# Kernel optimization log

Measured on AMD Instinct MI355X. Metric: run time of the kernel, lower is better.

The kernel has to match this reference:

```python
import jax, jax.numpy as jnp
import numpy as np
from jax import lax

KS = 7; KC = 64; S = 31; B = 1; H = 128; W = 128; ITERS = 3
LAM = 0.1   # Softshrink lambda
EPS = 1e-5  # BatchNorm eps


def conv2d(x, w, b):
    # x: [N,C,H,W], w: [O,C,kh,kw], b: [O]; stride 1, SAME padding (ks odd)
    y = lax.conv_general_dilated(x, w, (1, 1), 'SAME',
                                 dimension_numbers=('NCHW', 'OIHW', 'NCHW'))
    return y + b[None, :, None, None]


def band_conv(x5, w, b):
    # x5: [S,B,C,H,W] -> apply shared conv per band by merging S into batch
    s, bb, c, h, ww = x5.shape
    y = conv2d(x5.reshape(s * bb, c, h, ww), w, b)
    return y.reshape(s, bb, -1, h, ww)


def softshrink(x):
    return jnp.sign(x) * jnp.maximum(jnp.abs(x) - LAM, 0.0)


def setup_inputs() -> dict:
    key = jax.random.key(0)
    ks = jax.random.split(key, 12)
    sc = 0.05
    inputs = jax.random.normal(ks[0], (B, S, H, W), jnp.float32)
    W_fe   = jax.random.normal(ks[1], (KC, 1, KS, KS), jnp.float32) * sc
    b_fe   = jax.random.normal(ks[2], (KC,), jnp.float32) * sc
    W_enc  = jax.random.normal(ks[3], (ITERS, KC, 1, KS, KS), jnp.float32) * sc
    b_enc  = jax.random.normal(ks[4], (ITERS, KC), jnp.float32) * sc
    W_dec  = jax.random.normal(ks[5], (ITERS, 1, KC, KS, KS), jnp.float32) * sc
    b_dec  = jax.random.normal(ks[6], (ITERS, 1), jnp.float32) * sc
    W_last = jax.random.normal(ks[7], (1, KC, KS, KS), jnp.float32) * sc
    b_last = jax.random.normal(ks[8], (1,), jnp.float32) * sc
    W_z    = jax.random.normal(ks[9], (ITERS, KC, KC, KS, KS), jnp.float32) * sc
    b_z    = jax.random.normal(ks[10], (ITERS, KC), jnp.float32) * sc
    bn_gamma = jnp.ones((ITERS, KC), jnp.float32)
    bn_beta  = jnp.zeros((ITERS, KC), jnp.float32)
    return dict(inputs=inputs, W_fe=W_fe, b_fe=b_fe, W_enc=W_enc, b_enc=b_enc,
                W_dec=W_dec, b_dec=b_dec, W_last=W_last, b_last=b_last,
                W_z=W_z, b_z=b_z, bn_gamma=bn_gamma, bn_beta=bn_beta)


def reference(inputs, W_fe, b_fe, W_enc, b_enc, W_dec, b_dec,
              W_last, b_last, W_z, b_z, bn_gamma, bn_beta):
    # inputs: [B, S, H, W]; treat each band as [B,1,H,W]
    x = jnp.transpose(inputs, (1, 0, 2, 3))[:, :, None]  # [S,B,1,H,W]
    # initial sparse code per band (shared first encoder + softshrink)
    csc = softshrink(band_conv(x, W_fe, b_fe))            # [S,B,KC,H,W]

    for it in range(ITERS):
        lyr = it % ITERS  # cycle(range(_layers)) with _layers == ista_iters
        # per-band ISTA step (vectorized over bands)
        res = x - band_conv(csc, W_dec[lyr], b_dec[lyr])
        tmp = softshrink(csc + band_conv(res, W_enc[lyr], b_enc[lyr]))
        # GRU-style gate: sigmoid(BN(conv(tmp))); BN uses per-call (per-band)
        # batch statistics over (B,H,W) per channel, matching training mode
        zpre = band_conv(tmp, W_z[lyr], b_z[lyr])          # [S,B,KC,H,W]
        mu = jnp.mean(zpre, axis=(1, 3, 4), keepdims=True)
        var = jnp.var(zpre, axis=(1, 3, 4), keepdims=True)
        zn = (zpre - mu) * lax.rsqrt(var + EPS)
        g = bn_gamma[lyr][None, None, :, None, None]
        be = bn_beta[lyr][None, None, :, None, None]
        z = jax.nn.sigmoid(zn * g + be)
        # direction alternates: even iters sweep bands forward, odd backward
        fwd = (it % 2 == 0)
        t = tmp if fwd else tmp[::-1]
        zz = z if fwd else z[::-1]

        def step(carry, inp):
            ti, zi = inp
            new = zi * carry + (1.0 - zi) * ti
            return new, new

        _, ys = lax.scan(step, t[0], (t[1:], zz[1:]))
        seq = jnp.concatenate([t[:1], ys], axis=0)
        csc = seq if fwd else seq[::-1]

    out = band_conv(csc, W_last, b_last)[:, :, 0]  # [S,B,H,W]
    outputs = jnp.transpose(out, (1, 0, 2, 3))     # [B,S,H,W]
    return (csc, outputs)
```

## Files before the change

kernel.cpp:

```cpp
#include <hip/hip_runtime.h>
#include <hip/hip_bf16.h>
#include <math.h>

#define S31   31
#define KC    64
#define KS    7
#define KK    49
#define IMG   128
#define HW    16384
#define LAM   0.1f
#define BNEPS 1e-5f

#define PLSTRIDE 3872

#define TW    32
#define TH    8
#define DTW   38
#define DTH   14
#define DTILE 532

typedef __attribute__((ext_vector_type(8))) short  frag8;
typedef __attribute__((ext_vector_type(4))) float  facc4;

static __device__ __forceinline__ short f2bf(float f) {
    union { float f; unsigned u; } x; x.f = f;
    unsigned r = x.u + 0x7fffu + ((x.u >> 16) & 1u);
    return (short)(r >> 16);
}

__global__ void reorder_weights(const float* __restrict__ Wz,
                                const float* __restrict__ Wenc,
                                const float* __restrict__ Wfe,
                                short* __restrict__ wz_frag,
                                float* __restrict__ wenc_r,
                                float* __restrict__ wfe_r,
                                float* __restrict__ pstats) {
    int tid = blockIdx.x * 256 + threadIdx.x;
    const int NZ = 3 * KK * 4096;
    const int NE = 3 * KK * KC;
    const int NF = KK * KC;
    const int NP = 2 * S31 * KC;
    if (tid < NZ) {
        int j    = tid & 7;
        int lane = (tid >> 3) & 63;
        int og   = (tid >> 9) & 3;
        int ks   = (tid >> 11) & 1;
        int rem  = tid >> 12;
        int khkw = rem % KK;
        int lyr  = rem / KK;
        int ic = ks * 32 + ((lane >> 4) << 3) + j;
        int oc = (og << 4) + (lane & 15);
        float w = Wz[(((size_t)lyr * KC + oc) * KC + ic) * KK + khkw];
        wz_frag[tid] = f2bf(w);
    } else if (tid < NZ + NE) {
        int t = tid - NZ;
        int oc = t & 63;
        int kk = t >> 6;
        int k  = kk % KK;
        int lyr = kk / KK;
        wenc_r[t] = Wenc[((size_t)lyr * KC + oc) * KK + k];
    } else if (tid < NZ + NE + NF) {
        int t = tid - NZ - NE;
        int oc = t & 63;
        int k  = t >> 6;
        wfe_r[t] = Wfe[oc * KK + k];
    } else if (tid < NZ + NE + NF + NP) {
        pstats[tid - NZ - NE - NF] = 0.f;
    }
}

__global__ __launch_bounds__(256) void conv1to64(
        const float* __restrict__ src,
        const float* __restrict__ wr,
        const float* __restrict__ bias,
        const float* __restrict__ addsrc,
        float* __restrict__ dst,
        short* __restrict__ dst_t)
{
    int s    = blockIdx.y;
    int half = blockIdx.x & 1;
    int tile = blockIdx.x >> 1;
    int t    = threadIdx.x;
    int tx = t & 31, ty = t >> 5;
    int w0 = (tile & 3) << 5, h0 = (tile >> 2) << 3;

    __shared__ float t_s[DTILE];
    const float* sp = src + (size_t)s * HW;
    for (int i = threadIdx.x; i < DTILE; i += 256) {
        int r = i / DTW, c = i - r * DTW;
        int hh = h0 - 3 + r, ww = w0 - 3 + c;
        t_s[i] = (hh >= 0 && hh < IMG && ww >= 0 && ww < IMG) ? sp[hh * IMG + ww] : 0.f;
    }
    __syncthreads();

    int pix = (h0 + ty) * IMG + (w0 + tx);
    size_t base = ((size_t)s * KC + half * 32) * HW + pix;

    float addv[32];
    if (addsrc) {
#pragma unroll
        for (int i = 0; i < 32; i++) addv[i] = addsrc[base + (size_t)i * HW];
    } else {
#pragma unroll
        for (int i = 0; i < 32; i++) addv[i] = 0.f;
    }
    __builtin_amdgcn_sched_barrier(0);

    float acc[32];
#pragma unroll
    for (int i = 0; i < 32; i++) acc[i] = 0.f;

    const float* wrh = wr + half * 32;
#pragma unroll 1
    for (int kh = 0; kh < KS; kh++) {
#pragma unroll
        for (int kw = 0; kw < KS; kw++) {
            float v = t_s[(ty + kh) * DTW + tx + kw];
            const float* wk = wrh + (kh * KS + kw) * KC;
#pragma unroll
            for (int i = 0; i < 32; i++) acc[i] += v * wk[i];
        }
    }

    short* tb = dst_t ? (dst_t + (((size_t)half * S31 + s) * HW + pix) * 32) : nullptr;
#pragma unroll
    for (int g = 0; g < 4; g++) {
        frag8 vv;
#pragma unroll
        for (int j = 0; j < 8; j++) {
            int i = g * 8 + j;
            float v = acc[i] + bias[half * 32 + i];
            v += addv[i];
            v = (v > LAM) ? (v - LAM) : ((v < -LAM) ? (v + LAM) : 0.f);
            dst[base + (size_t)i * HW] = v;
            vv[j] = f2bf(v);
        }
        if (tb) *(frag8*)(tb + g * 8) = vv;
    }
}

#define ICB   4
#define CHUNK (ICB * DTILE)

__global__ __launch_bounds__(256) void conv64to1(
        const float* __restrict__ src,
        const float* __restrict__ w,
        const float* __restrict__ bias,
        const float* __restrict__ xsub,
        float* __restrict__ dst)
{
    int s    = blockIdx.y;
    int tile = blockIdx.x;
    int tx = threadIdx.x & 31, ty = threadIdx.x >> 5;
    int w0 = (tile & 3) << 5, h0 = (tile >> 2) << 3;

    __shared__ float t_s[2][CHUNK];

    int  goff[9];
    bool okf[9];
#pragma unroll
    for (int r = 0; r < 9; r++) {
        int j = threadIdx.x + r * 256;
        if (j < CHUNK) {
            int plane = j / DTILE, p = j - plane * DTILE;
            int rr = p / DTW, cc = p - rr * DTW;
            int hh = h0 - 3 + rr, ww = w0 - 3 + cc;
            bool inb = (hh >= 0 && hh < IMG && ww >= 0 && ww < IMG);
            goff[r] = plane * HW + (inb ? (hh * IMG + ww) : 0);
            okf[r]  = inb;
        }
    }

    const float* sbase = src + (size_t)s * KC * HW;

    float ldv[9];
#pragma unroll
    for (int r = 0; r < 9; r++)
        if (threadIdx.x + r * 256 < CHUNK)
            ldv[r] = okf[r] ? sbase[goff[r]] : 0.f;
#pragma unroll
    for (int r = 0; r < 9; r++)
        if (threadIdx.x + r * 256 < CHUNK)
            t_s[0][threadIdx.x + r * 256] = ldv[r];

    float acc = 0.f;
    __syncthreads();

#pragma unroll 1
    for (int blk = 0; blk < 16; blk++) {
        int cur = blk & 1;
        if (blk < 15) {
            const float* nb = sbase + (size_t)(blk + 1) * ICB * HW;
#pragma unroll
            for (int r = 0; r < 9; r++)
                if (threadIdx.x + r * 256 < CHUNK)
                    ldv[r] = okf[r] ? nb[goff[r]] : 0.f;
        }
        __builtin_amdgcn_sched_barrier(0);
#pragma unroll
        for (int pl = 0; pl < ICB; pl++) {
            int ic = blk * ICB + pl;
            const float* wk = w + ic * KK;
            const float* ts = &t_s[cur][pl * DTILE];
#pragma unroll 1
            for (int kh = 0; kh < KS; kh++) {
#pragma unroll
                for (int kw = 0; kw < KS; kw++)
                    acc += ts[(ty + kh) * DTW + tx + kw] * wk[kh * KS + kw];
            }
        }
        __syncthreads();
        if (blk < 15) {
#pragma unroll
            for (int r = 0; r < 9; r++)
                if (threadIdx.x + r * 256 < CHUNK)
                    t_s[cur ^ 1][threadIdx.x + r * 256] = ldv[r];
            __syncthreads();
        }
    }

    float v = acc + bias[0];
    int pix = (h0 + ty) * IMG + (w0 + tx);
    if (xsub) v = xsub[(size_t)s * HW + pix] - v;
    dst[(size_t)s * HW + pix] = v;
}

__global__ __launch_bounds__(512, 4) void conv_z_mfma(
        const short* __restrict__ srcT,
        const short* __restrict__ wfrag,
        const float* __restrict__ bias,
        float* __restrict__ dst,
        float* __restrict__ pstats)
{
    __shared__ __align__(16) short a_s[4 * PLSTRIDE];

    int s    = blockIdx.y;
    int tile = blockIdx.x;
    int h0 = (tile >> 3) << 4, w0 = (tile & 7) << 4;
    int tid  = threadIdx.x;
    int wave = tid >> 6, lane = tid & 63;
    int q = lane >> 4, m = lane & 15;

    facc4 acc[2][4];
#pragma unroll
    for (int i = 0; i < 2; i++)
#pragma unroll
        for (int j = 0; j < 4; j++)
            acc[i][j] = (facc4){0.f, 0.f, 0.f, 0.f};

#pragma unroll 1
    for (int pass = 0; pass < 2; ++pass) {
        if (pass) __syncthreads();

        const frag8* brow = (const frag8*)wfrag + (pass * 4) * 64 + lane;
        frag8 c0 = brow[0], c1 = brow[64], c2 = brow[128], c3 = brow[192];

        const short* tsrc = srcT + ((size_t)pass * S31 + s) * HW * 32;
        {
            int p = tid;
            if (p < 484) {
                int r = p / 22, c = p - r * 22;
                int hh = h0 - 3 + r, ww = w0 - 3 + c;
                bool ok = (hh >= 0 && hh < IMG && ww >= 0 && ww < IMG);
                const short* px = tsrc + (size_t)(ok ? (hh * IMG + ww) : 0) * 32;
                short* dp = a_s + p * 8;
#pragma unroll
                for (int c4 = 0; c4 < 4; c4++) {
                    frag8 v;
                    if (ok) v = *(const frag8*)(px + (c4 << 3));
                    else    v = (frag8)(short)0;
                    *(frag8*)(dp + c4 * PLSTRIDE) = v;
                }
            }
        }
        __syncthreads();

        const short* arow = a_s + q * PLSTRIDE + (wave * 2 * 22 + m) * 8;

#pragma unroll 1
        for (int kh = 0; kh < 7; ++kh) {
#pragma unroll
            for (int kw = 0; kw < 7; ++kw) {
                const frag8* bn = brow + (kw == 6 ? 7 : (kw + 1)) * 512;
                frag8 n0 = bn[0], n1 = bn[64], n2 = bn[128], n3 = bn[192];
                frag8 a0 = *(const frag8*)(arow + (0 * 22 + kw) * 8);
                frag8 a1 = *(const frag8*)(arow + (1 * 22 + kw) * 8);
                acc[0][0] = __builtin_amdgcn_mfma_f32_16x16x32_bf16(a0, c0, acc[0][0], 0, 0, 0);
                acc[0][1] = __builtin_amdgcn_mfma_f32_16x16x32_bf16(a0, c1, acc[0][1], 0, 0, 0);
                acc[0][2] = __builtin_amdgcn_mfma_f32_16x16x32_bf16(a0, c2, acc[0][2], 0, 0, 0);
                acc[0][3] = __builtin_amdgcn_mfma_f32_16x16x32_bf16(a0, c3, acc[0][3], 0, 0, 0);
                acc[1][0] = __builtin_amdgcn_mfma_f32_16x16x32_bf16(a1, c0, acc[1][0], 0, 0, 0);
                acc[1][1] = __builtin_amdgcn_mfma_f32_16x16x32_bf16(a1, c1, acc[1][1], 0, 0, 0);
                acc[1][2] = __builtin_amdgcn_mfma_f32_16x16x32_bf16(a1, c2, acc[1][2], 0, 0, 0);
                acc[1][3] = __builtin_amdgcn_mfma_f32_16x16x32_bf16(a1, c3, acc[1][3], 0, 0, 0);
                c0 = n0; c1 = n1; c2 = n2; c3 = n3;
            }
            arow += 22 * 8;
            brow += 7 * 512;
        }
    }

    int prow = h0 + wave * 2;
#pragma unroll
    for (int og = 0; og < 4; og++) {
        int oc = og * 16 + m;
        float bb = bias[oc];
        float s1 = 0.f, s2 = 0.f;
#pragma unroll
        for (int pg = 0; pg < 2; pg++) {
            float* dp = dst + ((size_t)s * KC + oc) * HW
                            + (size_t)(prow + pg) * IMG + w0 + q * 4;
            float4 v;
            v.x = acc[pg][og][0] + bb;
            v.y = acc[pg][og][1] + bb;
            v.z = acc[pg][og][2] + bb;
            v.w = acc[pg][og][3] + bb;
            s1 += v.x + v.y + v.z + v.w;
            s2 += v.x * v.x + v.y * v.y + v.z * v.z + v.w * v.w;
            *(float4*)dp = v;
        }
        s1 += __shfl_xor(s1, 16, 64); s2 += __shfl_xor(s2, 16, 64);
        s1 += __shfl_xor(s1, 32, 64); s2 += __shfl_xor(s2, 32, 64);
        if (q == 0) {
            atomicAdd(&pstats[(s * KC + oc) * 2],     s1);
            atomicAdd(&pstats[(s * KC + oc) * 2 + 1], s2);
        }
    }
}

__global__ __launch_bounds__(64) void bn_finalize(
        float* __restrict__ pstats,
        float* __restrict__ stats)
{
    int i = blockIdx.x * 64 + threadIdx.x;
    if (i < S31 * KC) {
        float s1 = pstats[i * 2], s2 = pstats[i * 2 + 1];
        pstats[i * 2] = 0.f;
        pstats[i * 2 + 1] = 0.f;
        float mu  = s1 * (1.f / HW);
        float var = s2 * (1.f / HW) - mu * mu;
        if (var < 0.f) var = 0.f;
        stats[i * 2]     = mu;
        stats[i * 2 + 1] = rsqrtf(var + BNEPS);
    }
}

__global__ __launch_bounds__(256) void band_scan(
        const float* __restrict__ tmp,
        const float* __restrict__ zpre,
        const float* __restrict__ stats,
        const float* __restrict__ gamma,
        const float* __restrict__ beta,
        float* __restrict__ csc,
        int fwd)
{
    int idx = blockIdx.x * 256 + threadIdx.x;
    int c = idx >> 14;
    float g = gamma[c], be = beta[c];
    float prev = 0.f;
    for (int step = 0; step < S31; step++) {
        int s = fwd ? step : (S31 - 1 - step);
        size_t off = (size_t)s * KC * HW + idx;
        float t  = tmp[off];
        float zp = zpre[off];
        float mu = stats[(s * KC + c) * 2];
        float rs = stats[(s * KC + c) * 2 + 1];
        float zn = (zp - mu) * rs * g + be;
        float z  = 1.f / (1.f + expf(-zn));
        float cur = (step == 0) ? t : (z * prev + (1.f - z) * t);
        csc[off] = cur;
        prev = cur;
    }
}

extern "C" void kernel_launch(void* const* d_in, const int* in_sizes, int n_in,
                              void* d_out, int out_size, void* d_ws, size_t ws_size,
                              hipStream_t stream) {
    const float* x      = (const float*)d_in[0];
    const float* W_fe   = (const float*)d_in[1];
    const float* b_fe   = (const float*)d_in[2];
    const float* W_enc  = (const float*)d_in[3];
    const float* b_enc  = (const float*)d_in[4];
    const float* W_dec  = (const float*)d_in[5];
    const float* b_dec  = (const float*)d_in[6];
    const float* W_last = (const float*)d_in[7];
    const float* b_last = (const float*)d_in[8];
    const float* W_z    = (const float*)d_in[9];
    const float* b_z    = (const float*)d_in[10];
    const float* bn_g   = (const float*)d_in[11];
    const float* bn_b   = (const float*)d_in[12];

    float* out     = (float*)d_out;
    float* csc     = out;
    float* outputs = out + (size_t)S31 * KC * HW;

    char* ws = (char*)d_ws;
    float* tmp     = (float*)ws; ws += (size_t)S31 * KC * HW * 4;
    float* zpre    = (float*)ws; ws += (size_t)S31 * KC * HW * 4;
    float* res     = (float*)ws; ws += (size_t)S31 * HW * 4;
    float* stats   = (float*)ws; ws += (size_t)S31 * KC * 2 * 4;
    float* pstats  = (float*)ws; ws += (size_t)S31 * KC * 2 * 4;
    short* wz_frag = (short*)ws; ws += ((size_t)3 * KK * 4096 + 4096) * 2;
    float* wenc_r  = (float*)ws; ws += (size_t)3 * KK * KC * 4;
    float* wfe_r   = (float*)ws; ws += (size_t)KK * KC * 4;
    short* tmp_t   = (short*)ws; ws += (size_t)2 * S31 * HW * 32 * 2;

    {
        int total = 3 * KK * 4096 + 3 * KK * KC + KK * KC + 2 * S31 * KC;
        reorder_weights<<<(total + 255) / 256, 256, 0, stream>>>(
            W_z, W_enc, W_fe, wz_frag, wenc_r, wfe_r, pstats);
    }

    dim3 gconv(64, S31);
    dim3 gconv2(128, S31);

    conv1to64<<<gconv2, 256, 0, stream>>>(x, wfe_r, b_fe, nullptr, csc, nullptr);

    for (int it = 0; it < 3; it++) {
        int lyr = it;
        conv64to1<<<gconv, 256, 0, stream>>>(
            csc, W_dec + (size_t)lyr * KC * KK, b_dec + lyr, x, res);
        conv1to64<<<gconv2, 256, 0, stream>>>(
            res, wenc_r + (size_t)lyr * KK * KC, b_enc + (size_t)lyr * KC, csc,
            tmp, tmp_t);
        conv_z_mfma<<<gconv, 512, 0, stream>>>(
            tmp_t, wz_frag + (size_t)lyr * KK * 4096, b_z + (size_t)lyr * KC,
            zpre, pstats);
        bn_finalize<<<S31, 64, 0, stream>>>(pstats, stats);
        band_scan<<<(KC * HW) / 256, 256, 0, stream>>>(
            tmp, zpre, stats, bn_g + (size_t)lyr * KC, bn_b + (size_t)lyr * KC,
            csc, (it % 2 == 0) ? 1 : 0);
    }

    conv64to1<<<gconv, 256, 0, stream>>>(csc, W_last, b_last, nullptr, outputs);
}
```

Measured before the change: 2.053 ms.

## Give each wave four pixel rows in conv_z MFMA and prefetch A fragments

The z-gate convolution block shrinks from 512 to 256 threads, and each wave now computes a 4x4 grid of 16x16 MFMA tiles (four pixel rows by four channel groups) instead of 2x4. Each weight fragment loaded from global memory is therefore reused across twice as many rows, and both the LDS A fragments and the B fragments are software-pipelined one step ahead. The aim is fewer weight loads per MFMA and better latency hiding. In exchange the kernel needs more accumulator and prefetch registers, and the launch bound drops to 3 blocks per CU with fewer waves per block, which lowers occupancy.

```diff
diff --git a/kernel.cpp b/kernel.cpp
--- a/kernel.cpp
+++ b/kernel.cpp
@@ -225,7 +225,7 @@
     dst[(size_t)s * HW + pix] = v;
 }
 
-__global__ __launch_bounds__(512, 4) void conv_z_mfma(
+__global__ __launch_bounds__(256, 3) void conv_z_mfma(
         const short* __restrict__ srcT,
         const short* __restrict__ wfrag,
         const float* __restrict__ bias,
@@ -241,9 +241,9 @@
     int wave = tid >> 6, lane = tid & 63;
     int q = lane >> 4, m = lane & 15;
 
-    facc4 acc[2][4];
-#pragma unroll
-    for (int i = 0; i < 2; i++)
+    facc4 acc[4][4];
+#pragma unroll
+    for (int i = 0; i < 4; i++)
 #pragma unroll
         for (int j = 0; j < 4; j++)
             acc[i][j] = (facc4){0.f, 0.f, 0.f, 0.f};
@@ -252,12 +252,10 @@
     for (int pass = 0; pass < 2; ++pass) {
         if (pass) __syncthreads();
 
-        const frag8* brow = (const frag8*)wfrag + (pass * 4) * 64 + lane;
-        frag8 c0 = brow[0], c1 = brow[64], c2 = brow[128], c3 = brow[192];
-
         const short* tsrc = srcT + ((size_t)pass * S31 + s) * HW * 32;
-        {
-            int p = tid;
+#pragma unroll
+        for (int rep = 0; rep < 2; rep++) {
+            int p = tid + rep * 256;
             if (p < 484) {
                 int r = p / 22, c = p - r * 22;
                 int hh = h0 - 3 + r, ww = w0 - 3 + c;
@@ -275,39 +273,60 @@
         }
         __syncthreads();
 
-        const short* arow = a_s + q * PLSTRIDE + (wave * 2 * 22 + m) * 8;
+        const short* arow = a_s + q * PLSTRIDE + (wave * 4 * 22 + m) * 8;
+        const frag8* brow = (const frag8*)wfrag + (pass * 4) * 64 + lane;
+
+        frag8 ca0 = *(const frag8*)(arow + (0 * 22) * 8);
+        frag8 ca1 = *(const frag8*)(arow + (1 * 22) * 8);
+        frag8 ca2 = *(const frag8*)(arow + (2 * 22) * 8);
+        frag8 ca3 = *(const frag8*)(arow + (3 * 22) * 8);
+        frag8 cb0 = brow[0], cb1 = brow[64], cb2 = brow[128], cb3 = brow[192];
 
 #pragma unroll 1
         for (int kh = 0; kh < 7; ++kh) {
+            const short* arow_n = (kh < 6) ? (arow + 22 * 8) : arow;
 #pragma unroll
             for (int kw = 0; kw < 7; ++kw) {
-                const frag8* bn = brow + (kw == 6 ? 7 : (kw + 1)) * 512;
-                frag8 n0 = bn[0], n1 = bn[64], n2 = bn[128], n3 = bn[192];
-                frag8 a0 = *(const frag8*)(arow + (0 * 22 + kw) * 8);
-                frag8 a1 = *(const frag8*)(arow + (1 * 22 + kw) * 8);
-                acc[0][0] = __builtin_amdgcn_mfma_f32_16x16x32_bf16(a0, c0, acc[0][0], 0, 0, 0);
-                acc[0][1] = __builtin_amdgcn_mfma_f32_16x16x32_bf16(a0, c1, acc[0][1], 0, 0, 0);
-                acc[0][2] = __builtin_amdgcn_mfma_f32_16x16x32_bf16(a0, c2, acc[0][2], 0, 0, 0);
-                acc[0][3] = __builtin_amdgcn_mfma_f32_16x16x32_bf16(a0, c3, acc[0][3], 0, 0, 0);
-                acc[1][0] = __builtin_amdgcn_mfma_f32_16x16x32_bf16(a1, c0, acc[1][0], 0, 0, 0);
-                acc[1][1] = __builtin_amdgcn_mfma_f32_16x16x32_bf16(a1, c1, acc[1][1], 0, 0, 0);
-                acc[1][2] = __builtin_amdgcn_mfma_f32_16x16x32_bf16(a1, c2, acc[1][2], 0, 0, 0);
-                acc[1][3] = __builtin_amdgcn_mfma_f32_16x16x32_bf16(a1, c3, acc[1][3], 0, 0, 0);
-                c0 = n0; c1 = n1; c2 = n2; c3 = n3;
+                const short* an = (kw < 6) ? arow : arow_n;
+                const int koff = (kw < 6) ? (kw + 1) : 0;
+                const frag8* bn = brow + (kw + 1) * 512;
+                frag8 na0 = *(const frag8*)(an + (0 * 22 + koff) * 8);
+                frag8 na1 = *(const frag8*)(an + (1 * 22 + koff) * 8);
+                frag8 na2 = *(const frag8*)(an + (2 * 22 + koff) * 8);
+                frag8 na3 = *(const frag8*)(an + (3 * 22 + koff) * 8);
+                frag8 nb0 = bn[0], nb1 = bn[64], nb2 = bn[128], nb3 = bn[192];
+                acc[0][0] = __builtin_amdgcn_mfma_f32_16x16x32_bf16(ca0, cb0, acc[0][0], 0, 0, 0);
+                acc[0][1] = __builtin_amdgcn_mfma_f32_16x16x32_bf16(ca0, cb1, acc[0][1], 0, 0, 0);
+                acc[0][2] = __builtin_amdgcn_mfma_f32_16x16x32_bf16(ca0, cb2, acc[0][2], 0, 0, 0);
+                acc[0][3] = __builtin_amdgcn_mfma_f32_16x16x32_bf16(ca0, cb3, acc[0][3], 0, 0, 0);
+                acc[1][0] = __builtin_amdgcn_mfma_f32_16x16x32_bf16(ca1, cb0, acc[1][0], 0, 0, 0);
+                acc[1][1] = __builtin_amdgcn_mfma_f32_16x16x32_bf16(ca1, cb1, acc[1][1], 0, 0, 0);
+                acc[1][2] = __builtin_amdgcn_mfma_f32_16x16x32_bf16(ca1, cb2, acc[1][2], 0, 0, 0);
+                acc[1][3] = __builtin_amdgcn_mfma_f32_16x16x32_bf16(ca1, cb3, acc[1][3], 0, 0, 0);
+                acc[2][0] = __builtin_amdgcn_mfma_f32_16x16x32_bf16(ca2, cb0, acc[2][0], 0, 0, 0);
+                acc[2][1] = __builtin_amdgcn_mfma_f32_16x16x32_bf16(ca2, cb1, acc[2][1], 0, 0, 0);
+                acc[2][2] = __builtin_amdgcn_mfma_f32_16x16x32_bf16(ca2, cb2, acc[2][2], 0, 0, 0);
+                acc[2][3] = __builtin_amdgcn_mfma_f32_16x16x32_bf16(ca2, cb3, acc[2][3], 0, 0, 0);
+                acc[3][0] = __builtin_amdgcn_mfma_f32_16x16x32_bf16(ca3, cb0, acc[3][0], 0, 0, 0);
+                acc[3][1] = __builtin_amdgcn_mfma_f32_16x16x32_bf16(ca3, cb1, acc[3][1], 0, 0, 0);
+                acc[3][2] = __builtin_amdgcn_mfma_f32_16x16x32_bf16(ca3, cb2, acc[3][2], 0, 0, 0);
+                acc[3][3] = __builtin_amdgcn_mfma_f32_16x16x32_bf16(ca3, cb3, acc[3][3], 0, 0, 0);
+                ca0 = na0; ca1 = na1; ca2 = na2; ca3 = na3;
+                cb0 = nb0; cb1 = nb1; cb2 = nb2; cb3 = nb3;
             }
             arow += 22 * 8;
             brow += 7 * 512;
         }
     }
 
-    int prow = h0 + wave * 2;
+    int prow = h0 + wave * 4;
 #pragma unroll
     for (int og = 0; og < 4; og++) {
         int oc = og * 16 + m;
         float bb = bias[oc];
         float s1 = 0.f, s2 = 0.f;
 #pragma unroll
-        for (int pg = 0; pg < 2; pg++) {
+        for (int pg = 0; pg < 4; pg++) {
             float* dp = dst + ((size_t)s * KC + oc) * HW
                             + (size_t)(prow + pg) * IMG + w0 + q * 4;
             float4 v;
@@ -423,7 +442,7 @@
         conv1to64<<<gconv2, 256, 0, stream>>>(
             res, wenc_r + (size_t)lyr * KK * KC, b_enc + (size_t)lyr * KC, csc,
             tmp, tmp_t);
-        conv_z_mfma<<<gconv, 512, 0, stream>>>(
+        conv_z_mfma<<<gconv, 256, 0, stream>>>(
             tmp_t, wz_frag + (size_t)lyr * KK * 4096, b_z + (size_t)lyr * KC,
             zpre, pstats);
         bn_finalize<<<S31, 64, 0, stream>>>(pstats, stats);
```

After: 1.749 ms. 1.17x faster.

## Give each wave four output rows in z-conv and reuse A fragments across kh

Applied to the files above, without the earlier changes.

The z-gate MFMA conv now runs 256 threads per block, and each wave computes four output rows instead of two, doubling the accumulators. The loop order is swapped to kw-outer, kh-inner, so A fragments slide through a four-register window with one new LDS load per kh. B weight fragments are prefetched two steps ahead. This cuts LDS reads and weight loads per MFMA, at the cost of higher register pressure and fewer waves per block.

```diff
diff --git a/kernel.cpp b/kernel.cpp
--- a/kernel.cpp
+++ b/kernel.cpp
@@ -225,7 +225,7 @@
     dst[(size_t)s * HW + pix] = v;
 }
 
-__global__ __launch_bounds__(512, 4) void conv_z_mfma(
+__global__ __launch_bounds__(256, 3) void conv_z_mfma(
         const short* __restrict__ srcT,
         const short* __restrict__ wfrag,
         const float* __restrict__ bias,
@@ -241,9 +241,9 @@
     int wave = tid >> 6, lane = tid & 63;
     int q = lane >> 4, m = lane & 15;
 
-    facc4 acc[2][4];
-#pragma unroll
-    for (int i = 0; i < 2; i++)
+    facc4 acc[4][4];
+#pragma unroll
+    for (int i = 0; i < 4; i++)
 #pragma unroll
         for (int j = 0; j < 4; j++)
             acc[i][j] = (facc4){0.f, 0.f, 0.f, 0.f};
@@ -252,12 +252,10 @@
     for (int pass = 0; pass < 2; ++pass) {
         if (pass) __syncthreads();
 
-        const frag8* brow = (const frag8*)wfrag + (pass * 4) * 64 + lane;
-        frag8 c0 = brow[0], c1 = brow[64], c2 = brow[128], c3 = brow[192];
-
         const short* tsrc = srcT + ((size_t)pass * S31 + s) * HW * 32;
-        {
-            int p = tid;
+#pragma unroll
+        for (int rep = 0; rep < 2; rep++) {
+            int p = tid + rep * 256;
             if (p < 484) {
                 int r = p / 22, c = p - r * 22;
                 int hh = h0 - 3 + r, ww = w0 - 3 + c;
@@ -275,16 +273,30 @@
         }
         __syncthreads();
 
-        const short* arow = a_s + q * PLSTRIDE + (wave * 2 * 22 + m) * 8;
+        const frag8* bbase = (const frag8*)wfrag + (pass * 4) * 64 + lane;
 
 #pragma unroll 1
-        for (int kh = 0; kh < 7; ++kh) {
-#pragma unroll
-            for (int kw = 0; kw < 7; ++kw) {
-                const frag8* bn = brow + (kw == 6 ? 7 : (kw + 1)) * 512;
-                frag8 n0 = bn[0], n1 = bn[64], n2 = bn[128], n3 = bn[192];
-                frag8 a0 = *(const frag8*)(arow + (0 * 22 + kw) * 8);
-                frag8 a1 = *(const frag8*)(arow + (1 * 22 + kw) * 8);
+        for (int kw = 0; kw < 7; ++kw) {
+            const short* acol = a_s + q * PLSTRIDE + (wave * 4 * 22 + m + kw) * 8;
+            const frag8* bk = bbase + kw * 512;
+
+            frag8 a0 = *(const frag8*)(acol + 0 * 176);
+            frag8 a1 = *(const frag8*)(acol + 1 * 176);
+            frag8 a2 = *(const frag8*)(acol + 2 * 176);
+            frag8 a3 = *(const frag8*)(acol + 3 * 176);
+            frag8 c0 = bk[0], c1 = bk[64], c2 = bk[128], c3 = bk[192];
+            const frag8* bk1 = bk + 7 * 512;
+            frag8 n0 = bk1[0], n1 = bk1[64], n2 = bk1[128], n3 = bk1[192];
+
+#pragma unroll
+            for (int kh = 0; kh < 7; ++kh) {
+                frag8 p0, p1, p2, p3;
+                if (kh < 5) {
+                    const frag8* bk2 = bk + (kh + 2) * (7 * 512);
+                    p0 = bk2[0]; p1 = bk2[64]; p2 = bk2[128]; p3 = bk2[192];
+                }
+                frag8 an;
+                if (kh < 6) an = *(const frag8*)(acol + (kh + 4) * 176);
                 acc[0][0] = __builtin_amdgcn_mfma_f32_16x16x32_bf16(a0, c0, acc[0][0], 0, 0, 0);
                 acc[0][1] = __builtin_amdgcn_mfma_f32_16x16x32_bf16(a0, c1, acc[0][1], 0, 0, 0);
                 acc[0][2] = __builtin_amdgcn_mfma_f32_16x16x32_bf16(a0, c2, acc[0][2], 0, 0, 0);
@@ -293,21 +305,30 @@
                 acc[1][1] = __builtin_amdgcn_mfma_f32_16x16x32_bf16(a1, c1, acc[1][1], 0, 0, 0);
                 acc[1][2] = __builtin_amdgcn_mfma_f32_16x16x32_bf16(a1, c2, acc[1][2], 0, 0, 0);
                 acc[1][3] = __builtin_amdgcn_mfma_f32_16x16x32_bf16(a1, c3, acc[1][3], 0, 0, 0);
+                acc[2][0] = __builtin_amdgcn_mfma_f32_16x16x32_bf16(a2, c0, acc[2][0], 0, 0, 0);
+                acc[2][1] = __builtin_amdgcn_mfma_f32_16x16x32_bf16(a2, c1, acc[2][1], 0, 0, 0);
+                acc[2][2] = __builtin_amdgcn_mfma_f32_16x16x32_bf16(a2, c2, acc[2][2], 0, 0, 0);
+                acc[2][3] = __builtin_amdgcn_mfma_f32_16x16x32_bf16(a2, c3, acc[2][3], 0, 0, 0);
+                acc[3][0] = __builtin_amdgcn_mfma_f32_16x16x32_bf16(a3, c0, acc[3][0], 0, 0, 0);
+                acc[3][1] = __builtin_amdgcn_mfma_f32_16x16x32_bf16(a3, c1, acc[3][1], 0, 0, 0);
+                acc[3][2] = __builtin_amdgcn_mfma_f32_16x16x32_bf16(a3, c2, acc[3][2], 0, 0, 0);
+                acc[3][3] = __builtin_amdgcn_mfma_f32_16x16x32_bf16(a3, c3, acc[3][3], 0, 0, 0);
+                a0 = a1; a1 = a2; a2 = a3;
+                if (kh < 6) a3 = an;
                 c0 = n0; c1 = n1; c2 = n2; c3 = n3;
+                if (kh < 5) { n0 = p0; n1 = p1; n2 = p2; n3 = p3; }
             }
-            arow += 22 * 8;
-            brow += 7 * 512;
-        }
-    }
-
-    int prow = h0 + wave * 2;
+        }
+    }
+
+    int prow = h0 + wave * 4;
 #pragma unroll
     for (int og = 0; og < 4; og++) {
         int oc = og * 16 + m;
         float bb = bias[oc];
         float s1 = 0.f, s2 = 0.f;
 #pragma unroll
-        for (int pg = 0; pg < 2; pg++) {
+        for (int pg = 0; pg < 4; pg++) {
             float* dp = dst + ((size_t)s * KC + oc) * HW
                             + (size_t)(prow + pg) * IMG + w0 + q * 4;
             float4 v;
@@ -423,7 +444,7 @@
         conv1to64<<<gconv2, 256, 0, stream>>>(
             res, wenc_r + (size_t)lyr * KK * KC, b_enc + (size_t)lyr * KC, csc,
             tmp, tmp_t);
-        conv_z_mfma<<<gconv, 512, 0, stream>>>(
+        conv_z_mfma<<<gconv, 256, 0, stream>>>(
             tmp_t, wz_frag + (size_t)lyr * KK * 4096, b_z + (size_t)lyr * KC,
             zpre, pstats);
         bn_finalize<<<S31, 64, 0, stream>>>(pstats, stats);
```

Result: faster. 1.729 ms (-15.8%).
